# Kernel tuning notes

Hardware: AMD Instinct MI355X
Metric: run time of the kernel (lower is better)

The kernel has to match this reference:

```python
import jax, jax.numpy as jnp
import numpy as np
import math

N_CELLS = 65536
HIDDEN = 128
IN_DIM = 64
MAX_DEG = 6
BOND_P = 0.5


def _build_graph():
    """2D lattice bond percolation -> padded adjacency [n, MAX_DEG] + signs + mask."""
    rng = np.random.default_rng(0)
    side = int(math.ceil(math.sqrt(N_CELLS)))
    adj = [[] for _ in range(N_CELLS)]
    for i in range(N_CELLS):
        col = i % side
        r = i + 1
        if col + 1 < side and r < N_CELLS and rng.random() < BOND_P:
            adj[i].append(r); adj[r].append(i)
        d = i + side
        if d < N_CELLS and rng.random() < BOND_P:
            adj[i].append(d); adj[d].append(i)
    for i in range(N_CELLS):  # ring fix for isolated nodes
        if not adj[i]:
            r = (i + 1) % N_CELLS
            adj[i].append(r); adj[r].append(i)
    sign_map = {}
    for i in range(N_CELLS):
        for j in adj[i]:
            key = (min(i, j), max(i, j))
            if key not in sign_map:
                sign_map[key] = 1.0 if rng.random() > 0.5 else -1.0
    nbr = np.zeros((N_CELLS, MAX_DEG), np.int32)
    sgn = np.ones((N_CELLS, MAX_DEG), np.float32)
    msk = np.zeros((N_CELLS, MAX_DEG), bool)
    for i in range(N_CELLS):
        for k, j in enumerate(adj[i][:MAX_DEG]):
            nbr[i, k] = j
            msk[i, k] = True
            sgn[i, k] = sign_map[(min(i, j), max(i, j))]
    return nbr, sgn, msk


def setup_inputs() -> dict:
    key = jax.random.key(0)
    ks = jax.random.split(key, 8)
    nbr, sgn, msk = _build_graph()
    n = N_CELLS
    cell_amp = jax.random.uniform(ks[0], (n, HIDDEN)) * 0.5 + 0.5
    cell_phase = jax.random.normal(ks[1], (n, HIDDEN)) * 0.5 \
        + (2.0 * jnp.pi * jnp.arange(n, dtype=jnp.float32) / n)[:, None]
    phase_vel = jax.random.normal(ks[2], (n, HIDDEN)) * 0.05
    return {
        'x': jax.random.normal(ks[3], (1, IN_DIM)),
        'cell_amp': cell_amp.astype(jnp.float32),
        'cell_phase': cell_phase.astype(jnp.float32),
        'phase_vel': phase_vel.astype(jnp.float32),
        'nbr_idx': jnp.asarray(nbr),
        'nbr_sign': jnp.asarray(sgn),
        'nbr_mask': jnp.asarray(msk),
        'W_in': jax.random.normal(ks[4], (HIDDEN, IN_DIM)) * 0.05,
        'b_in': jax.random.normal(ks[5], (HIDDEN,)) * 0.05,
        'W_dec': jax.random.normal(ks[6], (IN_DIM, 2 * HIDDEN)) * 0.05,
        'b_dec': jax.random.normal(ks[7], (IN_DIM,)) * 0.05,
        'step': 1,
    }


def reference(x, cell_amp, cell_phase, phase_vel, nbr_idx, nbr_sign, nbr_mask,
              W_in, b_in, W_dec, b_dec, step):
    n, h = cell_amp.shape
    # complex cell states, then phase-velocity rotation
    states = (cell_amp * jnp.exp(1j * cell_phase)).astype(jnp.complex64)
    states = states * jnp.exp(1j * phase_vel * 0.1)
    ang = jnp.angle(states)                               # [n, h]

    # --- neighbor interference (vectorized gather over padded adjacency) ---
    nbr_states = states[nbr_idx]                          # [n, d, h]
    nbr_ang = ang[nbr_idx]                                # [n, d, h]
    coupling = jnp.cos(ang[:, None, :] - nbr_ang) * nbr_sign[:, :, None]
    contrib = jnp.where(nbr_mask[:, :, None], coupling * nbr_states * 0.1, 0.0)
    interference = contrib.sum(axis=1)                    # [n, h]
    deg = nbr_mask.sum(axis=-1)                           # [n]
    new = 0.7 * states + 0.3 * interference / jnp.maximum(deg, 1)[:, None]
    new = jnp.where((deg > 0)[:, None], new, states)      # 'continue' for isolated nodes

    # --- morphism toward strongest neighbor (argmax over neighbors) ---
    strength = jnp.abs(states).sum(axis=-1)               # [n]
    nstr = jnp.where(nbr_mask, strength[nbr_idx], -jnp.inf)
    best_slot = jnp.argmax(nstr, axis=1)                  # first max, like python max()
    best = jnp.take_along_axis(nbr_idx, best_slot[:, None], axis=1)[:, 0]
    src = states[best]                                    # [n, h]
    morph = jnp.abs(src) * jnp.exp(1j * (jnp.angle(new) - jnp.angle(src)))
    new = jnp.where((deg >= 2)[:, None], new + 0.02 * morph, new)

    # --- global traveling wave ---
    t = step * 0.1
    wave = 0.02 * jnp.sin(t + 2.0 * jnp.pi * jnp.arange(n, dtype=jnp.float32) / n)
    new = new * (1.0 + wave)[:, None]

    # --- input-driven phase perturbation on first 32 cells ---
    sig = x[0] @ W_in.T + b_in                            # [h]
    pp = sig / (jnp.abs(sig).max() + 1e-8) * jnp.pi * 0.1
    idx = jnp.arange(n, dtype=jnp.float32)
    factor = jnp.where(jnp.arange(n) < 32, 0.1 / (1.0 + 0.1 * idx), 0.0)
    new_ang = jnp.angle(new) + pp[None, :] * factor[:, None]
    new = jnp.abs(new) * jnp.exp(1j * new_ang)

    # --- amplitude renormalization per cell ---
    amp = jnp.abs(new)
    amp = amp / (amp.max(axis=-1, keepdims=True) + 1e-8)
    cs = (amp * jnp.exp(1j * jnp.angle(new))).astype(jnp.complex64)

    # --- readout ---
    mean_state = cs.mean(axis=0)                          # [h]
    out_real = jnp.concatenate([mean_state.real, mean_state.imag])[None, :]
    pred = out_real @ W_dec.T + b_dec                     # [1, IN_DIM]
    tension = jnp.var(jnp.abs(cs), ddof=1)                # torch.var (unbiased)
    return pred, tension
```

## Files before the change

kernel.cpp:

```cpp
#include <hip/hip_runtime.h>
#include <hip/hip_fp16.h>
#include <math.h>

#define N_CELLS 65536
#define HIDDEN  128
#define IN_DIM  64
#define MAX_DEG 6

#define WPB    4
#define NPB    32
#define NBLK   (N_CELLS/NPB)
#define CHUNK  4
#define NXCD   8

#define INV2PI 0.15915494309189535f

__device__ __forceinline__ void fsincos(float x, float& s, float& c) {
    const float r = x * INV2PI;
    s = __builtin_amdgcn_sinf(r);
    c = __builtin_amdgcn_cosf(r);
}

#define WS_PP    0
#define WS_FLAG  512
#define WS_STR   1024
#define WS_T     (1024 + N_CELLS*4)
#define WS_ADJ   (WS_T + (size_t)N_CELLS*512)
#define WS_P     (WS_ADJ + (size_t)N_CELLS*32)
#define WS_SA    (WS_P + 256*NBLK*4)
#define WS_SA2   (WS_SA + NBLK*4)
#define WS_MEAN  (WS_SA2 + NBLK*4)

__global__ __launch_bounds__(256) void k_pre(
    const float* __restrict__ amp, const float* __restrict__ phase,
    const float* __restrict__ vel,
    const float* __restrict__ x, const float* __restrict__ W_in,
    const float* __restrict__ b_in, const unsigned char* __restrict__ maskb,
    int4* __restrict__ T, float* __restrict__ strength,
    float* __restrict__ pp, int* __restrict__ flag)
{
    const int tid = threadIdx.x;
    const int bx  = blockIdx.x;
    if (bx < N_CELLS/8) {
        const int blkp = (bx & (NXCD-1)) * (N_CELLS/8/NXCD) + (bx >> 3);
        const int node = blkp*8 + (tid >> 5);
        const int hl   = tid & 31;
        const size_t ro = (size_t)node*HIDDEN + 4*hl;
        const float4 a = *(const float4*)(amp   + ro);
        const float4 p = *(const float4*)(phase + ro);
        const float4 v = *(const float4*)(vel   + ro);
        union { int4 v4; __half2 h[4]; } tt;
        tt.h[0] = __floats2half2_rn(fmaf(0.1f, v.x, p.x), a.x);
        tt.h[1] = __floats2half2_rn(fmaf(0.1f, v.y, p.y), a.y);
        tt.h[2] = __floats2half2_rn(fmaf(0.1f, v.z, p.z), a.z);
        tt.h[3] = __floats2half2_rn(fmaf(0.1f, v.w, p.w), a.w);
        T[(size_t)node*32 + hl] = tt.v4;
        float st = a.x + a.y + a.z + a.w;
        #pragma unroll
        for (int off = 16; off > 0; off >>= 1) st += __shfl_xor(st, off);
        if (hl == 0) strength[node] = st;
        return;
    }
    __shared__ float sig[HIDDEN];
    __shared__ float red[HIDDEN];
    __shared__ int fl[256];
    if (tid < HIDDEN) {
        float acc = b_in[tid];
        #pragma unroll 8
        for (int d = 0; d < IN_DIM; ++d) acc = fmaf(W_in[tid*IN_DIM + d], x[d], acc);
        sig[tid] = acc;
        red[tid] = fabsf(acc);
    }
    int v = 0;
    #pragma unroll
    for (int r = 0; r < 4; ++r) v |= (int)maskb[(tid + 256*r)*4 + 1];
    fl[tid] = v;
    __syncthreads();
    for (int s = 64; s > 0; s >>= 1) {
        if (tid < s) red[tid] = fmaxf(red[tid], red[tid + s]);
        __syncthreads();
    }
    for (int s = 128; s > 0; s >>= 1) {
        if (tid < s) fl[tid] |= fl[tid + s];
        __syncthreads();
    }
    if (tid < HIDDEN) pp[tid] = sig[tid] / (red[0] + 1e-8f) * 0.314159265358979f;
    if (tid == 0) *flag = (fl[0] != 0) ? 1 : 0;
}

__global__ __launch_bounds__(256) void k_adj(
    const int* __restrict__ nbr_idx, const float* __restrict__ nbr_sign,
    const void* __restrict__ nbr_mask, const int* __restrict__ flagp,
    const float* __restrict__ strength, int4* __restrict__ adj)
{
    __shared__ int   lw[256][MAX_DEG];
    __shared__ float ls[256][MAX_DEG];
    __shared__ int   ldeg[256];
    const int t = threadIdx.x;
    const int bx = blockIdx.x;
    const int blkp = (bx & (NXCD-1)) * (N_CELLS/256/NXCD) + (bx >> 3);
    const int i = blkp*256 + t;
    const int flagv = *flagp;
    const unsigned char* mb = (const unsigned char*)nbr_mask;
    const int*           mi = (const int*)nbr_mask;
    int cnt = 0;
    #pragma unroll
    for (int k = 0; k < MAX_DEG; ++k) {
        const int e = i*MAX_DEG + k;
        const int m = flagv ? (mb[e] != 0) : (mi[e] != 0);
        const int j = nbr_idx[e];
        const float sg = nbr_sign[e];
        if (m) {
            lw[t][cnt] = j | ((sg < 0.0f) ? (1<<24) : 0) | (1<<25);
            ls[t][cnt] = strength[j];
            ++cnt;
        }
    }
    int cb = 0; float bv = ls[t][0];
    #pragma unroll
    for (int k = 1; k < MAX_DEG; ++k)
        if (k < cnt && ls[t][k] > bv) { bv = ls[t][k]; cb = k; }
    if (cb != 0) {
        const int tmp = lw[t][0];
        lw[t][0] = lw[t][cb];
        lw[t][cb] = tmp;
    }
    #pragma unroll
    for (int k = 0; k < MAX_DEG; ++k) if (k >= cnt) lw[t][k] = i;
    ldeg[t] = cnt;
    __syncthreads();
    const int kmax = max(cnt, ldeg[t ^ 1]);
    adj[2*(size_t)i    ] = make_int4(lw[t][0], lw[t][1], lw[t][2], lw[t][3]);
    adj[2*(size_t)i + 1] = make_int4(lw[t][4], lw[t][5], cnt, kmax);
}

__global__ __launch_bounds__(256) void k_mainc(
    const int4* __restrict__ T, const int4* __restrict__ adj,
    const int* __restrict__ step, const float* __restrict__ pp,
    float* __restrict__ P, float* __restrict__ p_sa, float* __restrict__ p_sa2)
{
    __shared__ float4 lredre[WPB][32], lredim[WPB][32];
    __shared__ float  lsa[WPB], lsa2[WPB];

    const int tid   = threadIdx.x;
    const int bx    = blockIdx.x;
    const int blk   = (bx & (NXCD-1)) * (NBLK/NXCD) + (bx >> 3);
    const int node0 = blk * NPB;

    const int wv   = tid >> 6;
    const int lane = tid & 63;
    const int half = lane >> 5;
    const int lh   = lane & 31;
    const float trev = 0.1f * (float)step[0] * INV2PI;
    const float4 ppv = ((const float4*)pp)[lh];

    float accre[4] = {0,0,0,0}, accim[4] = {0,0,0,0};
    float accsa = 0.f, accsa2 = 0.f;

    const int nlbase = wv*(2*CHUNK) + half;
    int4 A0n = adj[2*(size_t)(node0 + nlbase)    ];
    int4 A1n = adj[2*(size_t)(node0 + nlbase) + 1];

    #pragma unroll 1
    for (int c = 0; c < CHUNK; ++c) {
        const int nl = nlbase + 2*c;
        const int i  = node0 + nl;
        const int4 A0 = A0n, A1 = A1n;
        if (c + 1 < CHUNK) {
            A0n = adj[2*(size_t)(i + 2)    ];
            A1n = adj[2*(size_t)(i + 2) + 1];
        }
        const int deg  = A1.z;
        const int kmax = __builtin_amdgcn_readfirstlane(A1.w);
        const int slots[MAX_DEG] = {A0.x, A0.y, A0.z, A0.w, A1.x, A1.y};

        union HT { int4 v4; __half2 h[4]; };
        HT st, nt[MAX_DEG];
        st.v4 = T[(size_t)(unsigned)i*32 + lh];
        #pragma unroll
        for (int k = 0; k < MAX_DEG; ++k)
            if (k < kmax) nt[k].v4 = T[(size_t)(unsigned)(slots[k] & 0xFFFF)*32 + lh];

        float ci[4], si[4], ai[4];
        #pragma unroll
        for (int q = 0; q < 4; ++q) {
            const float2 tq = __half22float2(st.h[q]);
            fsincos(tq.x, si[q], ci[q]);
            ai[q] = tq.y;
        }

        float ir[4] = {0,0,0,0}, ii[4] = {0,0,0,0};
        float cb[4], sb[4], ab[4];
        #pragma unroll
        for (int k = 0; k < MAX_DEG; ++k) {
            if (k < kmax) {
                const int w = slots[k];
                const float vf = (float)((w >> 25) & 1);
                const float sgnm = (w & (1<<24)) ? -vf : vf;
                #pragma unroll
                for (int q = 0; q < 4; ++q) {
                    const float2 tq = __half22float2(nt[k].h[q]);
                    float cj, sj;
                    fsincos(tq.x, sj, cj);
                    const float cosD = ci[q]*cj + si[q]*sj;
                    const float m = cosD * sgnm * tq.y;
                    ir[q] = fmaf(m, cj, ir[q]);
                    ii[q] = fmaf(m, sj, ii[q]);
                    if (k == 0) { cb[q] = cj; sb[q] = sj; ab[q] = tq.y; }
                }
            }
        }

        const float f = 0.03f * __builtin_amdgcn_rcpf((float)deg);
        float nr[4], ni[4];
        #pragma unroll
        for (int q = 0; q < 4; ++q) {
            const float w7 = 0.7f * ai[q];
            nr[q] = fmaf(w7, ci[q], f*ir[q]);
            ni[q] = fmaf(w7, si[q], f*ii[q]);
        }

        const float g2 = (deg >= 2) ? 0.02f : 0.0f;
        #pragma unroll
        for (int q = 0; q < 4; ++q) {
            const float ex = ab[q]*cb[q], ey = ab[q]*sb[q];
            const float im = g2 * __builtin_amdgcn_rsqf(
                fmaxf(nr[q]*nr[q] + ni[q]*ni[q], 1e-30f));
            const float mr = im*(nr[q]*ex + ni[q]*ey);
            const float mi = im*(ni[q]*ex - nr[q]*ey);
            nr[q] += mr; ni[q] += mi;
        }

        const float wr = fmaf((float)i, 1.52587890625e-5f, trev);
        const float wf = 1.0f + 0.02f * __builtin_amdgcn_sinf(wr);
        #pragma unroll
        for (int q = 0; q < 4; ++q) { nr[q] *= wf; ni[q] *= wf; }

        if (i < 32) {
            const float fac = 0.1f / fmaf(0.1f, (float)i, 1.0f);
            const float pv[4] = {ppv.x, ppv.y, ppv.z, ppv.w};
            #pragma unroll
            for (int q = 0; q < 4; ++q) {
                float sp, cp;
                fsincos(pv[q]*fac, sp, cp);
                const float tr = nr[q]*cp - ni[q]*sp;
                ni[q] = ni[q]*cp + nr[q]*sp;
                nr[q] = tr;
            }
        }

        float m[4];
        #pragma unroll
        for (int q = 0; q < 4; ++q) m[q] = sqrtf(nr[q]*nr[q] + ni[q]*ni[q]);
        float lm = fmaxf(fmaxf(m[0], m[1]), fmaxf(m[2], m[3]));
        #pragma unroll
        for (int off = 16; off > 0; off >>= 1) lm = fmaxf(lm, __shfl_xor(lm, off));
        const float sc = 1.0f / (lm + 1e-8f);
        #pragma unroll
        for (int q = 0; q < 4; ++q) {
            accre[q] += nr[q]*sc;
            accim[q] += ni[q]*sc;
            const float Av = m[q]*sc;
            accsa  += Av;
            accsa2 += Av*Av;
        }
    }

    #pragma unroll
    for (int q = 0; q < 4; ++q) {
        accre[q] += __shfl_xor(accre[q], 32);
        accim[q] += __shfl_xor(accim[q], 32);
    }
    #pragma unroll
    for (int off = 32; off > 0; off >>= 1) {
        accsa  += __shfl_xor(accsa,  off);
        accsa2 += __shfl_xor(accsa2, off);
    }
    if (half == 0) {
        lredre[wv][lh] = make_float4(accre[0], accre[1], accre[2], accre[3]);
        lredim[wv][lh] = make_float4(accim[0], accim[1], accim[2], accim[3]);
    }
    if (lane == 0) { lsa[wv] = accsa; lsa2[wv] = accsa2; }
    __syncthreads();
    if (tid < 32) {
        float4 r = lredre[0][tid], im = lredim[0][tid];
        #pragma unroll
        for (int w = 1; w < WPB; ++w) {
            const float4 a = lredre[w][tid], b = lredim[w][tid];
            r.x += a.x; r.y += a.y; r.z += a.z; r.w += a.w;
            im.x += b.x; im.y += b.y; im.z += b.z; im.w += b.w;
        }
        P[(4*tid  )*NBLK + blk]       = r.x;
        P[(4*tid+1)*NBLK + blk]       = r.y;
        P[(4*tid+2)*NBLK + blk]       = r.z;
        P[(4*tid+3)*NBLK + blk]       = r.w;
        P[(128+4*tid  )*NBLK + blk]   = im.x;
        P[(128+4*tid+1)*NBLK + blk]   = im.y;
        P[(128+4*tid+2)*NBLK + blk]   = im.z;
        P[(128+4*tid+3)*NBLK + blk]   = im.w;
    }
    if (tid == 0) {
        p_sa [blk] = lsa[0]  + lsa[1]  + lsa[2]  + lsa[3];
        p_sa2[blk] = lsa2[0] + lsa2[1] + lsa2[2] + lsa2[3];
    }
}

__global__ void k_red(const float* __restrict__ P, float* __restrict__ mean)
{
    __shared__ double red[256];
    const int r = blockIdx.x, tid = threadIdx.x;
    double s = 0.0;
    #pragma unroll
    for (int k = 0; k < NBLK/256; ++k) s += (double)P[(size_t)r*NBLK + tid + 256*k];
    red[tid] = s;
    __syncthreads();
    for (int st = 128; st > 0; st >>= 1) { if (tid < st) red[tid] += red[tid + st]; __syncthreads(); }
    if (tid == 0) mean[r] = (float)(red[0] / (double)N_CELLS);
}

__global__ void k_final(const float* __restrict__ mean_in,
                        const float* __restrict__ p_sa, const float* __restrict__ p_sa2,
                        const float* __restrict__ W_dec, const float* __restrict__ b_dec,
                        float* __restrict__ out)
{
    __shared__ float  mean[2*HIDDEN];
    __shared__ double dred[256];
    __shared__ double tots[2];
    const int tid = threadIdx.x;
    mean[tid] = mean_in[tid];
    double sa = 0.0, sa2 = 0.0;
    #pragma unroll
    for (int k = 0; k < NBLK/256; ++k) {
        sa  += (double)p_sa [tid + 256*k];
        sa2 += (double)p_sa2[tid + 256*k];
    }
    dred[tid] = sa;
    __syncthreads();
    for (int s = 128; s > 0; s >>= 1) { if (tid < s) dred[tid] += dred[tid + s]; __syncthreads(); }
    if (tid == 0) tots[0] = dred[0];
    __syncthreads();
    dred[tid] = sa2;
    __syncthreads();
    for (int s = 128; s > 0; s >>= 1) { if (tid < s) dred[tid] += dred[tid + s]; __syncthreads(); }
    if (tid == 0) tots[1] = dred[0];
    __syncthreads();

    if (tid < IN_DIM) {
        float acc = b_dec[tid];
        #pragma unroll 8
        for (int c = 0; c < 2*HIDDEN; ++c) acc = fmaf(mean[c], W_dec[tid*2*HIDDEN + c], acc);
        out[tid] = acc;
    }
    if (tid == 0) {
        const double M = (double)N_CELLS * (double)HIDDEN;
        const double var = (tots[1] - tots[0]*tots[0]/M) / (M - 1.0);
        out[IN_DIM] = (float)var;
    }
}

extern "C" void kernel_launch(void* const* d_in, const int* in_sizes, int n_in,
                              void* d_out, int out_size, void* d_ws, size_t ws_size,
                              hipStream_t stream)
{
    const float* x       = (const float*)d_in[0];
    const float* amp     = (const float*)d_in[1];
    const float* phase   = (const float*)d_in[2];
    const float* vel     = (const float*)d_in[3];
    const int*   nbr_idx = (const int*)d_in[4];
    const float* nbr_sgn = (const float*)d_in[5];
    const void*  nbr_msk = d_in[6];
    const float* W_in    = (const float*)d_in[7];
    const float* b_in    = (const float*)d_in[8];
    const float* W_dec   = (const float*)d_in[9];
    const float* b_dec   = (const float*)d_in[10];
    const int*   step    = (const int*)d_in[11];

    char* wsb = (char*)d_ws;
    float* pp    = (float*)(wsb + WS_PP);
    int*   flag  = (int*)  (wsb + WS_FLAG);
    float* strg  = (float*)(wsb + WS_STR);
    int4*  T     = (int4*) (wsb + WS_T);
    int4*  adjv  = (int4*) (wsb + WS_ADJ);
    float* P     = (float*)(wsb + WS_P);
    float* p_sa  = (float*)(wsb + WS_SA);
    float* p_sa2 = (float*)(wsb + WS_SA2);
    float* meanb = (float*)(wsb + WS_MEAN);
    float* out   = (float*)d_out;

    k_pre<<<N_CELLS/8 + 1, 256, 0, stream>>>(amp, phase, vel, x, W_in, b_in,
                                             (const unsigned char*)nbr_msk,
                                             T, strg, pp, flag);
    k_adj<<<N_CELLS/256, 256, 0, stream>>>(nbr_idx, nbr_sgn, nbr_msk, flag, strg, adjv);
    k_mainc<<<NBLK, 256, 0, stream>>>(T, adjv, step, pp, P, p_sa, p_sa2);
    k_red<<<256, 256, 0, stream>>>(P, meanb);
    k_final<<<1, 256, 0, stream>>>(meanb, p_sa, p_sa2, W_dec, b_dec, out);
}
```

Measured before the change: 69.76 us.

## Fuse all five kernels into one cooperative persistent kernel with grid syncs

Replaces the chain of five launches (pre, adjacency build, main gather, reduction, final) with a single cooperative kernel of 512 blocks that uses grid.sync between phases. Adjacency building is moved into shared memory per block, so the adj workspace is no longer written or re-read. Each block now handles 128 nodes instead of 32, and the reduction runs over 512 partials. The goal is to remove launch gaps and the global round trips for adjacency. In exchange it relies on grid-wide barriers and gives up occupancy and parallelism in the main gather phase, with the old launch chain kept as a fallback if the cooperative launch fails.

```diff
diff --git a/kernel.cpp b/kernel.cpp
--- a/kernel.cpp
+++ b/kernel.cpp
@@ -1,17 +1,24 @@
 #include <hip/hip_runtime.h>
 #include <hip/hip_fp16.h>
+#include <hip/hip_cooperative_groups.h>
 #include <math.h>
+
+namespace cg = cooperative_groups;
 
 #define N_CELLS 65536
 #define HIDDEN  128
 #define IN_DIM  64
 #define MAX_DEG 6
-
-#define WPB    4
-#define NPB    32
-#define NBLK   (N_CELLS/NPB)
-#define CHUNK  4
-#define NXCD   8
+#define NXCD    8
+
+#define NBLKF    512
+#define NODES_PB 128
+#define WPB      4
+#define CITER    16
+
+#define NPB_B    32
+#define NBLK_B   (N_CELLS/NPB_B)
+#define CHUNK_B  4
 
 #define INV2PI 0.15915494309189535f
 
@@ -27,9 +34,336 @@
 #define WS_T     (1024 + N_CELLS*4)
 #define WS_ADJ   (WS_T + (size_t)N_CELLS*512)
 #define WS_P     (WS_ADJ + (size_t)N_CELLS*32)
-#define WS_SA    (WS_P + 256*NBLK*4)
-#define WS_SA2   (WS_SA + NBLK*4)
-#define WS_MEAN  (WS_SA2 + NBLK*4)
+#define WS_SA    (WS_P + 256*NBLK_B*4)
+#define WS_SA2   (WS_SA + NBLK_B*4)
+#define WS_MEAN  (WS_SA2 + NBLK_B*4)
+
+__global__ __launch_bounds__(256, 2) void k_fused(
+    const float* __restrict__ amp, const float* __restrict__ phase,
+    const float* __restrict__ vel,
+    const float* __restrict__ x, const float* __restrict__ W_in,
+    const float* __restrict__ b_in, const unsigned char* __restrict__ maskb,
+    const int* __restrict__ nbr_idx, const float* __restrict__ nbr_sign,
+    const int* __restrict__ step,
+    int4* __restrict__ T, float* __restrict__ strength,
+    float* __restrict__ pp, int* __restrict__ flag,
+    float* __restrict__ P, float* __restrict__ p_sa, float* __restrict__ p_sa2,
+    float* __restrict__ meanb,
+    const float* __restrict__ W_dec, const float* __restrict__ b_dec,
+    float* __restrict__ out)
+{
+    cg::grid_group grid = cg::this_grid();
+
+    __shared__ int    law[NODES_PB][8];
+    __shared__ float  lsk[NODES_PB][MAX_DEG];
+    __shared__ int    kmx[NODES_PB/2];
+    __shared__ float4 lredre[WPB][32], lredim[WPB][32];
+    __shared__ float  lsa[WPB], lsa2[WPB];
+    __shared__ double dred[256];
+    __shared__ float  sreda[256];
+    __shared__ double tots[2];
+
+    const int tid = threadIdx.x;
+    const int bx  = blockIdx.x;
+    const int blk = (bx & (NXCD-1)) * (NBLKF/NXCD) + (bx >> 3);
+    const int node0 = blk * NODES_PB;
+
+    {
+        const int hw = tid >> 5;
+        const int hl = tid & 31;
+        #pragma unroll 4
+        for (int r = 0; r < NODES_PB/8; ++r) {
+            const int node = node0 + r*8 + hw;
+            const size_t ro = (size_t)node*HIDDEN + 4*hl;
+            const float4 a = *(const float4*)(amp   + ro);
+            const float4 p = *(const float4*)(phase + ro);
+            const float4 v = *(const float4*)(vel   + ro);
+            union { int4 v4; __half2 h[4]; } tt;
+            tt.h[0] = __floats2half2_rn(fmaf(0.1f, v.x, p.x), a.x);
+            tt.h[1] = __floats2half2_rn(fmaf(0.1f, v.y, p.y), a.y);
+            tt.h[2] = __floats2half2_rn(fmaf(0.1f, v.z, p.z), a.z);
+            tt.h[3] = __floats2half2_rn(fmaf(0.1f, v.w, p.w), a.w);
+            T[(size_t)node*32 + hl] = tt.v4;
+            float st = a.x + a.y + a.z + a.w;
+            #pragma unroll
+            for (int off = 16; off > 0; off >>= 1) st += __shfl_xor(st, off);
+            if (hl == 0) strength[node] = st;
+        }
+    }
+    if (bx == 0) {
+        if (tid < HIDDEN) {
+            float acc = b_in[tid];
+            #pragma unroll 8
+            for (int d = 0; d < IN_DIM; ++d) acc = fmaf(W_in[tid*IN_DIM + d], x[d], acc);
+            sreda[tid] = fabsf(acc);
+            ((float*)law)[tid] = acc;
+        }
+        int v = 0;
+        #pragma unroll
+        for (int r = 0; r < 4; ++r) v |= (int)maskb[(tid + 256*r)*4 + 1];
+        ((int*)lredre)[tid] = v;
+        __syncthreads();
+        for (int s = 64; s > 0; s >>= 1) {
+            if (tid < s) sreda[tid] = fmaxf(sreda[tid], sreda[tid + s]);
+            __syncthreads();
+        }
+        for (int s = 128; s > 0; s >>= 1) {
+            if (tid < s) ((int*)lredre)[tid] |= ((int*)lredre)[tid + s];
+            __syncthreads();
+        }
+        if (tid < HIDDEN)
+            pp[tid] = ((float*)law)[tid] / (sreda[0] + 1e-8f) * 0.314159265358979f;
+        if (tid == 0) *flag = (((int*)lredre)[0] != 0) ? 1 : 0;
+        __syncthreads();
+    }
+
+    grid.sync();
+
+    {
+        const int flagv = *flag;
+        const int* mi = (const int*)maskb;
+        for (int e0 = tid; e0 < NODES_PB*MAX_DEG; e0 += 256) {
+            const int n = e0 / MAX_DEG, k = e0 - n*MAX_DEG;
+            const int e = (node0 + n)*MAX_DEG + k;
+            const int m = flagv ? (maskb[e] != 0) : (mi[e] != 0);
+            const int j = nbr_idx[e];
+            const float sg = nbr_sign[e];
+            law[n][k] = m ? (j | ((sg < 0.0f) ? (1<<24) : 0) | (1<<25)) : 0;
+            lsk[n][k] = m ? strength[j] : -3.0e38f;
+        }
+        __syncthreads();
+        if (tid < NODES_PB) {
+            int w[MAX_DEG]; float s[MAX_DEG];
+            #pragma unroll
+            for (int k = 0; k < MAX_DEG; ++k) { w[k] = law[tid][k]; s[k] = lsk[tid][k]; }
+            int cw[MAX_DEG]; float cs[MAX_DEG]; int cnt = 0;
+            #pragma unroll
+            for (int k = 0; k < MAX_DEG; ++k)
+                if (w[k] >> 25) { cw[cnt] = w[k]; cs[cnt] = s[k]; ++cnt; }
+            int cb = 0; float bv = cs[0];
+            #pragma unroll
+            for (int k = 1; k < MAX_DEG; ++k)
+                if (k < cnt && cs[k] > bv) { bv = cs[k]; cb = k; }
+            const int tmp = cw[0]; cw[0] = cw[cb]; cw[cb] = tmp;
+            #pragma unroll
+            for (int k = 0; k < MAX_DEG; ++k)
+                if (k >= cnt) cw[k] = node0 + tid;
+            #pragma unroll
+            for (int k = 0; k < MAX_DEG; ++k) law[tid][k] = cw[k];
+            law[tid][6] = cnt;
+        }
+        __syncthreads();
+        if (tid < NODES_PB/2) kmx[tid] = max(law[2*tid][6], law[2*tid+1][6]);
+        __syncthreads();
+    }
+
+    const int wv   = tid >> 6;
+    const int lane = tid & 63;
+    const int half = lane >> 5;
+    const int lh   = lane & 31;
+    const float trev = 0.1f * (float)step[0] * INV2PI;
+    const float4 ppv = ((const float4*)pp)[lh];
+
+    float accre[4] = {0,0,0,0}, accim[4] = {0,0,0,0};
+    float accsa = 0.f, accsa2 = 0.f;
+
+    #pragma unroll 1
+    for (int c = 0; c < CITER; ++c) {
+        const int nl = wv*(2*CITER) + 2*c + half;
+        const int i  = node0 + nl;
+        const int deg  = law[nl][6];
+        const int kmax = __builtin_amdgcn_readfirstlane(kmx[wv*CITER + c]);
+        const int slots[MAX_DEG] = {law[nl][0], law[nl][1], law[nl][2],
+                                    law[nl][3], law[nl][4], law[nl][5]};
+
+        union HT { int4 v4; __half2 h[4]; };
+        HT st, nt[MAX_DEG];
+        st.v4 = T[(size_t)(unsigned)i*32 + lh];
+        #pragma unroll
+        for (int k = 0; k < MAX_DEG; ++k)
+            if (k < kmax) nt[k].v4 = T[(size_t)(unsigned)(slots[k] & 0xFFFF)*32 + lh];
+
+        float ci[4], si[4], ai[4];
+        #pragma unroll
+        for (int q = 0; q < 4; ++q) {
+            const float2 tq = __half22float2(st.h[q]);
+            fsincos(tq.x, si[q], ci[q]);
+            ai[q] = tq.y;
+        }
+
+        float ir[4] = {0,0,0,0}, ii[4] = {0,0,0,0};
+        float cb[4], sb[4], ab[4];
+        #pragma unroll
+        for (int k = 0; k < MAX_DEG; ++k) {
+            if (k < kmax) {
+                const int w = slots[k];
+                const float vf = (float)((w >> 25) & 1);
+                const float sgnm = (w & (1<<24)) ? -vf : vf;
+                #pragma unroll
+                for (int q = 0; q < 4; ++q) {
+                    const float2 tq = __half22float2(nt[k].h[q]);
+                    float cj, sj;
+                    fsincos(tq.x, sj, cj);
+                    const float cosD = ci[q]*cj + si[q]*sj;
+                    const float m = cosD * sgnm * tq.y;
+                    ir[q] = fmaf(m, cj, ir[q]);
+                    ii[q] = fmaf(m, sj, ii[q]);
+                    if (k == 0) { cb[q] = cj; sb[q] = sj; ab[q] = tq.y; }
+                }
+            }
+        }
+
+        const float f = 0.03f * __builtin_amdgcn_rcpf((float)deg);
+        float nr[4], ni[4];
+        #pragma unroll
+        for (int q = 0; q < 4; ++q) {
+            const float w7 = 0.7f * ai[q];
+            nr[q] = fmaf(w7, ci[q], f*ir[q]);
+            ni[q] = fmaf(w7, si[q], f*ii[q]);
+        }
+
+        const float g2 = (deg >= 2) ? 0.02f : 0.0f;
+        #pragma unroll
+        for (int q = 0; q < 4; ++q) {
+            const float ex = ab[q]*cb[q], ey = ab[q]*sb[q];
+            const float im = g2 * __builtin_amdgcn_rsqf(
+                fmaxf(nr[q]*nr[q] + ni[q]*ni[q], 1e-30f));
+            const float mr = im*(nr[q]*ex + ni[q]*ey);
+            const float mi = im*(ni[q]*ex - nr[q]*ey);
+            nr[q] += mr; ni[q] += mi;
+        }
+
+        const float wr = fmaf((float)i, 1.52587890625e-5f, trev);
+        const float wf = 1.0f + 0.02f * __builtin_amdgcn_sinf(wr);
+        #pragma unroll
+        for (int q = 0; q < 4; ++q) { nr[q] *= wf; ni[q] *= wf; }
+
+        if (i < 32) {
+            const float fac = 0.1f / fmaf(0.1f, (float)i, 1.0f);
+            const float pv[4] = {ppv.x, ppv.y, ppv.z, ppv.w};
+            #pragma unroll
+            for (int q = 0; q < 4; ++q) {
+                float sp, cp;
+                fsincos(pv[q]*fac, sp, cp);
+                const float tr = nr[q]*cp - ni[q]*sp;
+                ni[q] = ni[q]*cp + nr[q]*sp;
+                nr[q] = tr;
+            }
+        }
+
+        float m[4];
+        #pragma unroll
+        for (int q = 0; q < 4; ++q) m[q] = sqrtf(nr[q]*nr[q] + ni[q]*ni[q]);
+        float lm = fmaxf(fmaxf(m[0], m[1]), fmaxf(m[2], m[3]));
+        #pragma unroll
+        for (int off = 16; off > 0; off >>= 1) lm = fmaxf(lm, __shfl_xor(lm, off));
+        const float sc = 1.0f / (lm + 1e-8f);
+        #pragma unroll
+        for (int q = 0; q < 4; ++q) {
+            accre[q] += nr[q]*sc;
+            accim[q] += ni[q]*sc;
+            const float Av = m[q]*sc;
+            accsa  += Av;
+            accsa2 += Av*Av;
+        }
+    }
+
+    #pragma unroll
+    for (int q = 0; q < 4; ++q) {
+        accre[q] += __shfl_xor(accre[q], 32);
+        accim[q] += __shfl_xor(accim[q], 32);
+    }
+    #pragma unroll
+    for (int off = 32; off > 0; off >>= 1) {
+        accsa  += __shfl_xor(accsa,  off);
+        accsa2 += __shfl_xor(accsa2, off);
+    }
+    __syncthreads();
+    if (half == 0) {
+        lredre[wv][lh] = make_float4(accre[0], accre[1], accre[2], accre[3]);
+        lredim[wv][lh] = make_float4(accim[0], accim[1], accim[2], accim[3]);
+    }
+    if (lane == 0) { lsa[wv] = accsa; lsa2[wv] = accsa2; }
+    __syncthreads();
+    if (tid < 32) {
+        float4 r = lredre[0][tid], im = lredim[0][tid];
+        #pragma unroll
+        for (int w = 1; w < WPB; ++w) {
+            const float4 a = lredre[w][tid], b = lredim[w][tid];
+            r.x += a.x; r.y += a.y; r.z += a.z; r.w += a.w;
+            im.x += b.x; im.y += b.y; im.z += b.z; im.w += b.w;
+        }
+        P[(4*tid  )*NBLKF + blk]       = r.x;
+        P[(4*tid+1)*NBLKF + blk]       = r.y;
+        P[(4*tid+2)*NBLKF + blk]       = r.z;
+        P[(4*tid+3)*NBLKF + blk]       = r.w;
+        P[(128+4*tid  )*NBLKF + blk]   = im.x;
+        P[(128+4*tid+1)*NBLKF + blk]   = im.y;
+        P[(128+4*tid+2)*NBLKF + blk]   = im.z;
+        P[(128+4*tid+3)*NBLKF + blk]   = im.w;
+    }
+    if (tid == 0) {
+        p_sa [blk] = lsa[0]  + lsa[1]  + lsa[2]  + lsa[3];
+        p_sa2[blk] = lsa2[0] + lsa2[1] + lsa2[2] + lsa2[3];
+    }
+
+    grid.sync();
+
+    if (bx < 256) {
+        double s = 0.0;
+        #pragma unroll
+        for (int k = 0; k < NBLKF/256; ++k)
+            s += (double)P[(size_t)bx*NBLKF + tid + 256*k];
+        dred[tid] = s;
+        __syncthreads();
+        for (int st = 128; st > 0; st >>= 1) {
+            if (tid < st) dred[tid] += dred[tid + st];
+            __syncthreads();
+        }
+        if (tid == 0) meanb[bx] = (float)(dred[0] / (double)N_CELLS);
+    }
+
+    grid.sync();
+
+    if (bx == 0) {
+        sreda[tid] = meanb[tid];
+        double sa = 0.0, sa2 = 0.0;
+        #pragma unroll
+        for (int k = 0; k < NBLKF/256; ++k) {
+            sa  += (double)p_sa [tid + 256*k];
+            sa2 += (double)p_sa2[tid + 256*k];
+        }
+        dred[tid] = sa;
+        __syncthreads();
+        for (int s = 128; s > 0; s >>= 1) {
+            if (tid < s) dred[tid] += dred[tid + s];
+            __syncthreads();
+        }
+        if (tid == 0) tots[0] = dred[0];
+        __syncthreads();
+        dred[tid] = sa2;
+        __syncthreads();
+        for (int s = 128; s > 0; s >>= 1) {
+            if (tid < s) dred[tid] += dred[tid + s];
+            __syncthreads();
+        }
+        if (tid == 0) tots[1] = dred[0];
+        __syncthreads();
+
+        if (tid < IN_DIM) {
+            float acc = b_dec[tid];
+            #pragma unroll 8
+            for (int c = 0; c < 2*HIDDEN; ++c)
+                acc = fmaf(sreda[c], W_dec[tid*2*HIDDEN + c], acc);
+            out[tid] = acc;
+        }
+        if (tid == 0) {
+            const double M = (double)N_CELLS * (double)HIDDEN;
+            const double var = (tots[1] - tots[0]*tots[0]/M) / (M - 1.0);
+            out[IN_DIM] = (float)var;
+        }
+    }
+}
 
 __global__ __launch_bounds__(256) void k_pre(
     const float* __restrict__ amp, const float* __restrict__ phase,
@@ -144,8 +478,8 @@
 
     const int tid   = threadIdx.x;
     const int bx    = blockIdx.x;
-    const int blk   = (bx & (NXCD-1)) * (NBLK/NXCD) + (bx >> 3);
-    const int node0 = blk * NPB;
+    const int blk   = (bx & (NXCD-1)) * (NBLK_B/NXCD) + (bx >> 3);
+    const int node0 = blk * NPB_B;
 
     const int wv   = tid >> 6;
     const int lane = tid & 63;
@@ -157,16 +491,16 @@
     float accre[4] = {0,0,0,0}, accim[4] = {0,0,0,0};
     float accsa = 0.f, accsa2 = 0.f;
 
-    const int nlbase = wv*(2*CHUNK) + half;
+    const int nlbase = wv*(2*CHUNK_B) + half;
     int4 A0n = adj[2*(size_t)(node0 + nlbase)    ];
     int4 A1n = adj[2*(size_t)(node0 + nlbase) + 1];
 
     #pragma unroll 1
-    for (int c = 0; c < CHUNK; ++c) {
+    for (int c = 0; c < CHUNK_B; ++c) {
         const int nl = nlbase + 2*c;
         const int i  = node0 + nl;
         const int4 A0 = A0n, A1 = A1n;
-        if (c + 1 < CHUNK) {
+        if (c + 1 < CHUNK_B) {
             A0n = adj[2*(size_t)(i + 2)    ];
             A1n = adj[2*(size_t)(i + 2) + 1];
         }
@@ -290,14 +624,14 @@
             r.x += a.x; r.y += a.y; r.z += a.z; r.w += a.w;
             im.x += b.x; im.y += b.y; im.z += b.z; im.w += b.w;
         }
-        P[(4*tid  )*NBLK + blk]       = r.x;
-        P[(4*tid+1)*NBLK + blk]       = r.y;
-        P[(4*tid+2)*NBLK + blk]       = r.z;
-        P[(4*tid+3)*NBLK + blk]       = r.w;
-        P[(128+4*tid  )*NBLK + blk]   = im.x;
-        P[(128+4*tid+1)*NBLK + blk]   = im.y;
-        P[(128+4*tid+2)*NBLK + blk]   = im.z;
-        P[(128+4*tid+3)*NBLK + blk]   = im.w;
+        P[(4*tid  )*NBLK_B + blk]       = r.x;
+        P[(4*tid+1)*NBLK_B + blk]       = r.y;
+        P[(4*tid+2)*NBLK_B + blk]       = r.z;
+        P[(4*tid+3)*NBLK_B + blk]       = r.w;
+        P[(128+4*tid  )*NBLK_B + blk]   = im.x;
+        P[(128+4*tid+1)*NBLK_B + blk]   = im.y;
+        P[(128+4*tid+2)*NBLK_B + blk]   = im.z;
+        P[(128+4*tid+3)*NBLK_B + blk]   = im.w;
     }
     if (tid == 0) {
         p_sa [blk] = lsa[0]  + lsa[1]  + lsa[2]  + lsa[3];
@@ -311,7 +645,7 @@
     const int r = blockIdx.x, tid = threadIdx.x;
     double s = 0.0;
     #pragma unroll
-    for (int k = 0; k < NBLK/256; ++k) s += (double)P[(size_t)r*NBLK + tid + 256*k];
+    for (int k = 0; k < NBLK_B/256; ++k) s += (double)P[(size_t)r*NBLK_B + tid + 256*k];
     red[tid] = s;
     __syncthreads();
     for (int st = 128; st > 0; st >>= 1) { if (tid < st) red[tid] += red[tid + st]; __syncthreads(); }
@@ -330,7 +664,7 @@
     mean[tid] = mean_in[tid];
     double sa = 0.0, sa2 = 0.0;
     #pragma unroll
-    for (int k = 0; k < NBLK/256; ++k) {
+    for (int k = 0; k < NBLK_B/256; ++k) {
         sa  += (double)p_sa [tid + 256*k];
         sa2 += (double)p_sa2[tid + 256*k];
     }
@@ -364,7 +698,7 @@
 {
     const float* x       = (const float*)d_in[0];
     const float* amp     = (const float*)d_in[1];
-    const float* phase   = (const float*)d_in[2];
+    const float* phs     = (const float*)d_in[2];
     const float* vel     = (const float*)d_in[3];
     const int*   nbr_idx = (const int*)d_in[4];
     const float* nbr_sgn = (const float*)d_in[5];
@@ -387,11 +721,25 @@
     float* meanb = (float*)(wsb + WS_MEAN);
     float* out   = (float*)d_out;
 
-    k_pre<<<N_CELLS/8 + 1, 256, 0, stream>>>(amp, phase, vel, x, W_in, b_in,
-                                             (const unsigned char*)nbr_msk,
-                                             T, strg, pp, flag);
-    k_adj<<<N_CELLS/256, 256, 0, stream>>>(nbr_idx, nbr_sgn, nbr_msk, flag, strg, adjv);
-    k_mainc<<<NBLK, 256, 0, stream>>>(T, adjv, step, pp, P, p_sa, p_sa2);
-    k_red<<<256, 256, 0, stream>>>(P, meanb);
-    k_final<<<1, 256, 0, stream>>>(meanb, p_sa, p_sa2, W_dec, b_dec, out);
+    const unsigned char* maskb = (const unsigned char*)nbr_msk;
+
+    void* args[] = {
+        (void*)&amp, (void*)&phs, (void*)&vel,
+        (void*)&x, (void*)&W_in, (void*)&b_in, (void*)&maskb,
+        (void*)&nbr_idx, (void*)&nbr_sgn, (void*)&step,
+        (void*)&T, (void*)&strg, (void*)&pp, (void*)&flag,
+        (void*)&P, (void*)&p_sa, (void*)&p_sa2, (void*)&meanb,
+        (void*)&W_dec, (void*)&b_dec, (void*)&out
+    };
+    hipError_t err = hipLaunchCooperativeKernel((void*)k_fused, dim3(NBLKF),
+                                                dim3(256), args, 0, stream);
+    if (err != hipSuccess) {
+        k_pre<<<N_CELLS/8 + 1, 256, 0, stream>>>(amp, phs, vel, x, W_in, b_in,
+                                                 maskb, T, strg, pp, flag);
+        k_adj<<<N_CELLS/256, 256, 0, stream>>>(nbr_idx, nbr_sgn, nbr_msk, flag,
+                                               strg, adjv);
+        k_mainc<<<NBLK_B, 256, 0, stream>>>(T, adjv, step, pp, P, p_sa, p_sa2);
+        k_red<<<256, 256, 0, stream>>>(P, meanb);
+        k_final<<<1, 256, 0, stream>>>(meanb, p_sa, p_sa2, W_dec, b_dec, out);
+    }
 }
```

New measurement: 257.1 us. 3.69x slower.
